# Optimization experiments

Hardware: AMD Instinct MI355X
Metric: run time of the kernel (lower is better)

Reference implementation:

```python
import jax, jax.numpy as jnp
import numpy as np

N_WAY = 5
K_SHOT = 5
NBNN_TOPK = 3
TEMPERATURE = 2.0
EPS = 1e-8


def setup_inputs() -> dict:
    key = jax.random.key(0)
    k1, k2, k3 = jax.random.split(key, 3)
    b, q, c, h, w = 4, 75, 640, 11, 11
    s = N_WAY * K_SHOT
    support_xf = jax.random.normal(k1, (b, s, c, h, w), jnp.float32)
    query_xf = jax.random.normal(k2, (b, q, c, h, w), jnp.float32)
    # episodes are ordered class-major: [way0 shots..., way1 shots..., ...]
    support_y = jnp.tile(jnp.repeat(jnp.arange(N_WAY, dtype=jnp.int32), K_SHOT)[None, :], (b, 1))
    query_y = jax.random.randint(k3, (b, q), 0, N_WAY, dtype=jnp.int32)
    return {"support_xf": support_xf, "query_xf": query_xf,
            "support_y": support_y, "query_y": query_y}


def _mn4_loss(support_xf, query_xf, query_y):
    b, s, c, h, w = support_xf.shape
    q = query_xf.shape[1]
    M_q = h * w
    M_s = K_SHOT * h * w

    # ---- InnerproductSimilarity (cosine) ----
    # support: [b, N, c, M_s]  (class-major grouping of shots)
    sf = support_xf.reshape(b, N_WAY, K_SHOT, c, h * w).transpose(0, 1, 3, 2, 4).reshape(b, N_WAY, c, M_s)
    qf = query_xf.reshape(b, q, c, M_q)
    sf = sf / (jnp.linalg.norm(sf, axis=2, keepdims=True) + EPS)
    qf = qf / (jnp.linalg.norm(qf, axis=2, keepdims=True) + EPS)
    # simi: [b, q, N, M_q, M_s]
    simi = jnp.einsum('bqcm,bncs->bqnms', qf, sf)

    # ---- _MNN (compensate_for_single=True branch) ----
    # merged view: [b, q, M_q, N*M_s]
    merged = simi.transpose(0, 1, 3, 2, 4).reshape(b, q, M_q, N_WAY * M_s)
    query_nearest = jnp.argmax(merged, axis=-1)          # [b, q, M_q]
    class_wise_max = simi.max(-1).max(2) + 1.0           # [b, q, M_q]
    class_m = jax.nn.one_hot(query_nearest, N_WAY * M_s, dtype=simi.dtype) * class_wise_max[..., None]
    support_nearest = jnp.argmax(class_m, axis=-2)       # [b, q, N*M_s]
    gathered = jnp.take_along_axis(support_nearest, query_nearest, axis=-1)  # [b, q, M_q]
    q_mask = (gathered == jnp.arange(M_q)[None, None, :])                    # [b, q, M_q]

    # ---- NBNN value: topk over support descriptors, masked sum over query descriptors ----
    topv = jax.lax.top_k(simi, NBNN_TOPK)[0].mean(-1)    # [b, q, N, M_q]
    query_value = (topv * q_mask[:, :, None, :].astype(topv.dtype)).sum(-1)  # [b, q, N]
    logits = query_value.reshape(b * q, N_WAY) / TEMPERATURE

    # ---- cross entropy (mean) ----
    logp = jax.nn.log_softmax(logits, axis=-1)
    y = query_y.reshape(-1)
    loss = -jnp.take_along_axis(logp, y[:, None], axis=1).mean()
    return loss


def reference(support_xf, query_xf, support_y, query_y):
    del support_y  # episodes are class-major by construction
    return _mn4_loss(support_xf, query_xf, query_y)
```

## Files before the change

kernel.cpp:

```cpp
#include <hip/hip_runtime.h>
#include <hip/hip_bf16.h>
#include <math.h>

#define BB 4
#define QQ 75
#define NBQ 300
#define CC 640
#define HW 121
#define NW 5
#define KS 5
#define SS 25
#define MS 605
#define JT 3025
#define BQ_PER_XCD 38

typedef __attribute__((ext_vector_type(8))) short short8;
typedef __attribute__((ext_vector_type(4))) float f32x4;

#define OFF_SBF   0
#define SBF_F     (BB*JT*CC/2)
#define OFF_QBF   (OFF_SBF + SBF_F)
#define QBF_F     (NBQ*HW*CC/2)
#define OFF_P     (OFF_QBF + QBF_F)
#define OFF_NRM   OFF_P

__device__ __forceinline__ void async16(const void* g, void* l) {
    __builtin_amdgcn_global_load_lds(
        (const __attribute__((address_space(1))) unsigned int*)g,
        (__attribute__((address_space(3))) unsigned int*)l, 16, 0, 0);
}

__global__ void norm_kernel(const float* __restrict__ sup, const float* __restrict__ qry,
                            float* __restrict__ nrm, float* __restrict__ out)
{
    const int blk = blockIdx.x;
    const int col = blk >> 2, r = blk & 3;
    const int hw  = threadIdx.x;
    if (blk == 0 && hw == 0) out[0] = 0.f;
    const float* src = (col < BB * SS)
        ? sup + (size_t)col * (CC * HW)
        : qry + (size_t)(col - BB * SS) * (CC * HW);
    float ss = 0.f;
    if (hw < HW) {
        const float* p = src + hw;
#pragma unroll 16
        for (int i = 0; i < CC / 4; ++i) {
            const float v = p[(size_t)(r + i * 4) * HW];
            ss = fmaf(v, v, ss);
        }
    }
    nrm[((size_t)col * 4 + r) * 128 + hw] = ss;
}

__global__ void scale_kernel(const float* __restrict__ sup, const float* __restrict__ qry,
                             const float* __restrict__ nrm,
                             __hip_bfloat16* __restrict__ Sbf, __hip_bfloat16* __restrict__ Qbf)
{
    const int blk = blockIdx.x;
    const int col = blk >> 2, qtr = blk & 3;
    const int t   = threadIdx.x;
    const float* src;
    __hip_bfloat16* dst;
    if (col < BB * SS) {
        const int b = col / SS, s = col % SS;
        const int n = s / KS, k = s % KS;
        src = sup + (size_t)col * (CC * HW);
        dst = Sbf + ((size_t)b * JT + n * MS + k * HW) * CC;
    } else {
        const int bq = col - BB * SS;
        src = qry + (size_t)bq * (CC * HW);
        dst = Qbf + (size_t)bq * (HW * CC);
    }

    __shared__ float inv[128];
    __shared__ float T[32][128];

    if (t < 128) {
        const float p0 = nrm[((size_t)col * 4 + 0) * 128 + t];
        const float p1 = nrm[((size_t)col * 4 + 1) * 128 + t];
        const float p2 = nrm[((size_t)col * 4 + 2) * 128 + t];
        const float p3 = nrm[((size_t)col * 4 + 3) * 128 + t];
        inv[t] = (t < HW) ? 1.f / (sqrtf((p0 + p2) + (p1 + p3)) + 1e-8f) : 0.f;
    }

    for (int it = 0; it < 5; ++it) {
        const int c0 = qtr * 160 + it * 32;
        __syncthreads();
#pragma unroll
        for (int i = 0; i < 16; ++i) {
            int idx = t + i * 256;
            int cc = idx >> 7, hw = idx & 127;
            if (hw < HW) T[cc][hw] = src[(size_t)(c0 + cc) * HW + hw] * inv[hw];
        }
        __syncthreads();
        const int hw = t >> 1, half = t & 1;
        if (hw < HW) {
            __hip_bfloat16 hv[16];
#pragma unroll
            for (int i = 0; i < 16; ++i) hv[i] = __float2bfloat16(T[half * 16 + i][hw]);
            int4* op = reinterpret_cast<int4*>(dst + (size_t)hw * CC + c0 + half * 16);
            op[0] = reinterpret_cast<int4*>(hv)[0];
            op[1] = reinterpret_cast<int4*>(hv)[1];
        }
    }
}

__launch_bounds__(256, 3)
__global__ void simi_kernel(const __hip_bfloat16* __restrict__ Sbf,
                            const __hip_bfloat16* __restrict__ Qbf,
                            float4* __restrict__ pout)
{
    const int xcd   = blockIdx.x & 7;
    const int local = blockIdx.x >> 3;
    const int n     = local % NW;
    const int bq    = xcd * BQ_PER_XCD + local / NW;
    if (bq >= NBQ) return;
    const int b   = bq / QQ;
    const int tid = threadIdx.x;
    const int lane = tid & 63, wid = tid >> 6;
    const int l15 = lane & 15, l4 = lane >> 4;
    const int wj0 = (wid & 1) * 64;
    const int wm0 = (wid >> 1) * 64;

    const unsigned short* qbase = (const unsigned short*)(Qbf + (size_t)bq * (HW * CC));
    const unsigned short* sbase = (const unsigned short*)(Sbf + ((size_t)b * JT + n * MS) * CC);

    __shared__ __align__(16) unsigned short AsBuf[3][128 * 32];
    __shared__ __align__(16) unsigned short BsBuf[3][128 * 32];

    const int srow = lane >> 2;
    const int kb   = (lane & 3) ^ ((lane >> 3) & 3);
    int aoff2[2];
#pragma unroll
    for (int g = 0; g < 2; ++g) {
        int arow = wid * 32 + g * 16 + srow;
        int grow = arow < HW ? arow : HW - 1;
        aoff2[g] = grow * CC + kb * 8;
    }
    int jb2[2];
#pragma unroll
    for (int g = 0; g < 2; ++g) jb2[g] = wid * 32 + g * 16 + srow;

    const int ldso_base = wid * 2048 + lane * 16;

#define STAGE(ms0_, c0_, nb_)                                                        \
    {                                                                                \
        _Pragma("unroll")                                                            \
        for (int g = 0; g < 2; ++g) {                                                \
            const int ldso = ldso_base + g * 1024;                                   \
            async16(qbase + aoff2[g] + (c0_), (char*)&AsBuf[nb_][0] + ldso);         \
            int j_ = (ms0_) + jb2[g];                                                \
            int jc_ = j_ < MS ? j_ : MS - 1;                                         \
            async16(sbase + jc_ * CC + kb * 8 + (c0_), (char*)&BsBuf[nb_][0] + ldso);\
        }                                                                            \
    }

    float rt0[4], rt1[4], rt2[4]; int ra[4];
#pragma unroll
    for (int i = 0; i < 4; ++i) { rt0[i] = -INFINITY; rt1[i] = -INFINITY; rt2[i] = -INFINITY; ra[i] = 0; }

    f32x4 acc[4][4];
#pragma unroll
    for (int ji = 0; ji < 4; ++ji)
#pragma unroll
        for (int qi = 0; qi < 4; ++qi)
#pragma unroll
            for (int r = 0; r < 4; ++r) acc[ji][qi][r] = 0.f;

    STAGE(0, 0, 0);
    int nb = 0;

    const int slot = l4 ^ ((l15 >> 1) & 3);
    const int aro  = (wm0 + l15) * 32 + slot * 8;
    const int bro  = (wj0 + l15) * 32 + slot * 8;

    for (int t = 0; t < 100; ++t) {
        const int tn = t + 1;
        const int nxt = (nb == 2) ? 0 : nb + 1;
        if (tn < 100) {
            const int nms = (tn / 20) * 128;
            const int nc  = (tn % 20) * 32;
            STAGE(nms, nc, nxt);
            asm volatile("s_waitcnt vmcnt(4)" ::: "memory");
        } else {
            asm volatile("s_waitcnt vmcnt(0)" ::: "memory");
        }
        __builtin_amdgcn_s_barrier();

        short8 af[4], bf[4];
#pragma unroll
        for (int qi = 0; qi < 4; ++qi)
            af[qi] = *(const short8*)(&AsBuf[nb][0] + aro + qi * 512);
#pragma unroll
        for (int ji = 0; ji < 4; ++ji)
            bf[ji] = *(const short8*)(&BsBuf[nb][0] + bro + ji * 512);

        __builtin_amdgcn_s_setprio(1);
#pragma unroll
        for (int ji = 0; ji < 4; ++ji)
#pragma unroll
            for (int qi = 0; qi < 4; ++qi)
                acc[ji][qi] = __builtin_amdgcn_mfma_f32_16x16x32_bf16(
                    bf[ji], af[qi], acc[ji][qi], 0, 0, 0);
        __builtin_amdgcn_s_setprio(0);
        nb = nxt;

        if ((t % 20) == 19) {
            const int ms0 = (t / 20) * 128;
#pragma unroll
            for (int qi = 0; qi < 4; ++qi)
#pragma unroll
                for (int ji = 0; ji < 4; ++ji)
#pragma unroll
                    for (int r = 0; r < 4; ++r) {
                        const int jl = ms0 + wj0 + ji * 16 + l4 * 4 + r;
                        float v = (jl < MS) ? acc[ji][qi][r] : -INFINITY;
                        const bool gt = v > rt0[qi];
                        ra[qi] = gt ? (n * MS + jl) : ra[qi];
                        const float m1 = fminf(rt0[qi], v);
                        rt0[qi] = fmaxf(rt0[qi], v);
                        const float m2 = fminf(rt1[qi], m1);
                        rt1[qi] = fmaxf(rt1[qi], m1);
                        rt2[qi] = fmaxf(rt2[qi], m2);
                    }
#pragma unroll
            for (int ji = 0; ji < 4; ++ji)
#pragma unroll
                for (int qi = 0; qi < 4; ++qi)
#pragma unroll
                    for (int r = 0; r < 4; ++r) acc[ji][qi][r] = 0.f;
        }
    }

#pragma unroll
    for (int qi = 0; qi < 4; ++qi) {
#pragma unroll
        for (int mask = 16; mask <= 32; mask <<= 1) {
            const float o0 = __shfl_xor(rt0[qi], mask);
            const float o1 = __shfl_xor(rt1[qi], mask);
            const float o2 = __shfl_xor(rt2[qi], mask);
            const int   oa = __shfl_xor(ra[qi],  mask);
            const bool take = (o0 > rt0[qi]) || (o0 == rt0[qi] && oa < ra[qi]);
            ra[qi] = take ? oa : ra[qi];
            float m1 = fminf(rt0[qi], o0); rt0[qi] = fmaxf(rt0[qi], o0);
            float m2 = fminf(rt1[qi], m1); rt1[qi] = fmaxf(rt1[qi], m1);
            rt2[qi] = fmaxf(rt2[qi], m2);
            m1 = fminf(rt0[qi], o1); rt0[qi] = fmaxf(rt0[qi], o1);
            m2 = fminf(rt1[qi], m1); rt1[qi] = fmaxf(rt1[qi], m1);
            rt2[qi] = fmaxf(rt2[qi], m2);
            m1 = fminf(rt0[qi], o2); rt0[qi] = fmaxf(rt0[qi], o2);
            m2 = fminf(rt1[qi], m1); rt1[qi] = fmaxf(rt1[qi], m1);
            rt2[qi] = fmaxf(rt2[qi], m2);
        }
    }

    __syncthreads();
    float4* mbuf = (float4*)&AsBuf[0][0];
    if ((wid & 1) == 0 && l4 == 0) {
#pragma unroll
        for (int qi = 0; qi < 4; ++qi) {
            float4 v; v.x = rt0[qi]; v.y = rt1[qi]; v.z = rt2[qi];
            v.w = __int_as_float(ra[qi]);
            mbuf[wm0 + qi * 16 + l15] = v;
        }
    }
    __syncthreads();
    if ((wid & 1) == 1 && l4 == 0) {
#pragma unroll
        for (int qi = 0; qi < 4; ++qi) {
            const int m = wm0 + qi * 16 + l15;
            const float4 o = mbuf[m];
            const int oa = __float_as_int(o.w);
            float s0 = rt0[qi], s1 = rt1[qi], s2 = rt2[qi]; int sa = ra[qi];
            const bool take = (o.x > s0) || (o.x == s0 && oa < sa);
            sa = take ? oa : sa;
            float m1 = fminf(s0, o.x); s0 = fmaxf(s0, o.x);
            float m2 = fminf(s1, m1);  s1 = fmaxf(s1, m1);
            s2 = fmaxf(s2, m2);
            m1 = fminf(s0, o.y); s0 = fmaxf(s0, o.y);
            m2 = fminf(s1, m1);  s1 = fmaxf(s1, m1);
            s2 = fmaxf(s2, m2);
            m1 = fminf(s0, o.z); s0 = fmaxf(s0, o.z);
            m2 = fminf(s1, m1);  s1 = fmaxf(s1, m1);
            s2 = fmaxf(s2, m2);
            if (m < HW) {
                float4 v; v.x = s0; v.y = s1; v.z = s2; v.w = __int_as_float(sa);
                pout[(bq * NW + n) * HW + m] = v;
            }
        }
    }
#undef STAGE
}

__global__ void merge_kernel(const float4* __restrict__ pout, const int* __restrict__ qy,
                             float* __restrict__ out)
{
    const int bq  = blockIdx.x;
    const int tid = threadIdx.x;

    __shared__ float cw[128];
    __shared__ int   ag[128];
    __shared__ float tv[NW][128];
    __shared__ float maskf[128];
    __shared__ float lg[8];

    if (tid < HW) {
        float g0 = -INFINITY; int garg = 0;
#pragma unroll
        for (int n = 0; n < NW; ++n) {
            const float4 a = pout[(bq * NW + n) * HW + tid];
            if (a.x > g0) { g0 = a.x; garg = __float_as_int(a.w); }
            tv[n][tid] = (a.x + a.y + a.z) * (1.f / 3.f);
        }
        cw[tid] = g0 + 1.0f;
        ag[tid] = garg;
    }
    __syncthreads();
    if (tid < HW) {
        const float mycw = cw[tid];
        const int   myag = ag[tid];
        float ok = 1.f;
        for (int m2 = 0; m2 < HW; ++m2) {
            if (m2 == tid) continue;
            if (ag[m2] == myag) {
                float c2 = cw[m2];
                if (c2 > mycw || (c2 == mycw && m2 < tid)) ok = 0.f;
            }
        }
        maskf[tid] = ok;
    }
    __syncthreads();
    if (tid < NW) {
        float s = 0.f;
        for (int mq = 0; mq < HW; ++mq) s += maskf[mq] * tv[tid][mq];
        lg[tid] = s * 0.5f;
    }
    __syncthreads();
    if (tid == 0) {
        float m = lg[0];
#pragma unroll
        for (int n2 = 1; n2 < NW; ++n2) m = fmaxf(m, lg[n2]);
        float se = 0.f;
#pragma unroll
        for (int n2 = 0; n2 < NW; ++n2) se += expf(lg[n2] - m);
        int y = qy[bq];
        atomicAdd(out, -(lg[y] - m - logf(se)) * (1.f / NBQ));
    }
}

extern "C" void kernel_launch(void* const* d_in, const int* in_sizes, int n_in,
                              void* d_out, int out_size, void* d_ws, size_t ws_size,
                              hipStream_t stream)
{
    const float* sup = (const float*)d_in[0];
    const float* qry = (const float*)d_in[1];
    const int*   qy  = (const int*)d_in[3];
    float* out = (float*)d_out;
    float* ws  = (float*)d_ws;

    __hip_bfloat16* Sbf = (__hip_bfloat16*)(ws + OFF_SBF);
    __hip_bfloat16* Qbf = (__hip_bfloat16*)(ws + OFF_QBF);
    float4* pout = (float4*)(ws + OFF_P);
    float*  nrm  = (float*)(ws + OFF_NRM);

    hipLaunchKernelGGL(norm_kernel,  dim3((BB * SS + NBQ) * 4), dim3(128), 0, stream,
                       sup, qry, nrm, out);
    hipLaunchKernelGGL(scale_kernel, dim3((BB * SS + NBQ) * 4), dim3(256), 0, stream,
                       sup, qry, nrm, Sbf, Qbf);
    hipLaunchKernelGGL(simi_kernel, dim3(8 * BQ_PER_XCD * NW), dim3(256), 0, stream,
                       Sbf, Qbf, pout);
    hipLaunchKernelGGL(merge_kernel, dim3(NBQ), dim3(128), 0, stream, pout, qy, out);
}
```

Baseline: 402.3 us.

## Process two queries per block to share support tile loads

Result: faster. 393.2 us (-2.3%).

```diff
diff --git a/kernel.cpp b/kernel.cpp
--- a/kernel.cpp
+++ b/kernel.cpp
@@ -12,7 +12,8 @@
 #define SS 25
 #define MS 605
 #define JT 3025
-#define BQ_PER_XCD 38
+#define NPAIR 38
+#define PAIRS_PER_XCD 19
 
 typedef __attribute__((ext_vector_type(8))) short short8;
 typedef __attribute__((ext_vector_type(4))) float f32x4;
@@ -105,7 +106,7 @@
     }
 }
 
-__launch_bounds__(256, 3)
+__launch_bounds__(512, 4)
 __global__ void simi_kernel(const __hip_bfloat16* __restrict__ Sbf,
                             const __hip_bfloat16* __restrict__ Qbf,
                             float4* __restrict__ pout)
@@ -113,46 +114,50 @@
     const int xcd   = blockIdx.x & 7;
     const int local = blockIdx.x >> 3;
     const int n     = local % NW;
-    const int bq    = xcd * BQ_PER_XCD + local / NW;
-    if (bq >= NBQ) return;
-    const int b   = bq / QQ;
-    const int tid = threadIdx.x;
+    const int pair  = xcd * PAIRS_PER_XCD + local / NW;
+    const int b     = pair / NPAIR;
+    const int pi    = pair % NPAIR;
+    const bool dup  = (pi == NPAIR - 1);
+    const int q0    = 2 * pi;
+    const int q1    = dup ? q0 : q0 + 1;
+    const int bq0   = b * QQ + q0;
+    const int bq1   = b * QQ + q1;
+
+    const int tid  = threadIdx.x;
     const int lane = tid & 63, wid = tid >> 6;
     const int l15 = lane & 15, l4 = lane >> 4;
+    const int wm0 = (wid >> 1) * 64;
     const int wj0 = (wid & 1) * 64;
-    const int wm0 = (wid >> 1) * 64;
-
-    const unsigned short* qbase = (const unsigned short*)(Qbf + (size_t)bq * (HW * CC));
+
+    const unsigned short* qb0 = (const unsigned short*)(Qbf + (size_t)bq0 * (HW * CC));
+    const unsigned short* qb1 = (const unsigned short*)(Qbf + (size_t)bq1 * (HW * CC));
     const unsigned short* sbase = (const unsigned short*)(Sbf + ((size_t)b * JT + n * MS) * CC);
 
-    __shared__ __align__(16) unsigned short AsBuf[3][128 * 32];
+    __shared__ __align__(16) unsigned short AsBuf[3][256 * 32];
     __shared__ __align__(16) unsigned short BsBuf[3][128 * 32];
 
     const int srow = lane >> 2;
     const int kb   = (lane & 3) ^ ((lane >> 3) & 3);
-    int aoff2[2];
+
+    const unsigned short* aptr[2];
 #pragma unroll
     for (int g = 0; g < 2; ++g) {
         int arow = wid * 32 + g * 16 + srow;
-        int grow = arow < HW ? arow : HW - 1;
-        aoff2[g] = grow * CC + kb * 8;
-    }
-    int jb2[2];
-#pragma unroll
-    for (int g = 0; g < 2; ++g) jb2[g] = wid * 32 + g * 16 + srow;
-
-    const int ldso_base = wid * 2048 + lane * 16;
+        int ml = arow & 127; ml = ml < HW ? ml : HW - 1;
+        aptr[g] = ((arow >> 7) ? qb1 : qb0) + ml * CC + kb * 8;
+    }
+    const int jrow = wid * 16 + srow;
+    const int ldsoA0 = wid * 2048 + lane * 16;
+    const int ldsoA1 = ldsoA0 + 1024;
+    const int ldsoB  = wid * 1024 + lane * 16;
 
 #define STAGE(ms0_, c0_, nb_)                                                        \
     {                                                                                \
-        _Pragma("unroll")                                                            \
-        for (int g = 0; g < 2; ++g) {                                                \
-            const int ldso = ldso_base + g * 1024;                                   \
-            async16(qbase + aoff2[g] + (c0_), (char*)&AsBuf[nb_][0] + ldso);         \
-            int j_ = (ms0_) + jb2[g];                                                \
-            int jc_ = j_ < MS ? j_ : MS - 1;                                         \
-            async16(sbase + jc_ * CC + kb * 8 + (c0_), (char*)&BsBuf[nb_][0] + ldso);\
-        }                                                                            \
+        async16(aptr[0] + (c0_), (char*)&AsBuf[nb_][0] + ldsoA0);                    \
+        async16(aptr[1] + (c0_), (char*)&AsBuf[nb_][0] + ldsoA1);                    \
+        int j_ = (ms0_) + jrow;                                                      \
+        int jc_ = j_ < MS ? j_ : MS - 1;                                             \
+        async16(sbase + jc_ * CC + kb * 8 + (c0_), (char*)&BsBuf[nb_][0] + ldsoB);   \
     }
 
     float rt0[4], rt1[4], rt2[4]; int ra[4];
@@ -181,27 +186,29 @@
             const int nms = (tn / 20) * 128;
             const int nc  = (tn % 20) * 32;
             STAGE(nms, nc, nxt);
-            asm volatile("s_waitcnt vmcnt(4)" ::: "memory");
+            asm volatile("s_waitcnt vmcnt(3)" ::: "memory");
         } else {
             asm volatile("s_waitcnt vmcnt(0)" ::: "memory");
         }
         __builtin_amdgcn_s_barrier();
 
-        short8 af[4], bf[4];
+        short8 af[4];
 #pragma unroll
         for (int qi = 0; qi < 4; ++qi)
             af[qi] = *(const short8*)(&AsBuf[nb][0] + aro + qi * 512);
-#pragma unroll
-        for (int ji = 0; ji < 4; ++ji)
-            bf[ji] = *(const short8*)(&BsBuf[nb][0] + bro + ji * 512);
-
+
+        short8 bfA = *(const short8*)(&BsBuf[nb][0] + bro);
         __builtin_amdgcn_s_setprio(1);
 #pragma unroll
-        for (int ji = 0; ji < 4; ++ji)
+        for (int ji = 0; ji < 4; ++ji) {
+            short8 bfB;
+            if (ji < 3) bfB = *(const short8*)(&BsBuf[nb][0] + bro + (ji + 1) * 512);
 #pragma unroll
             for (int qi = 0; qi < 4; ++qi)
                 acc[ji][qi] = __builtin_amdgcn_mfma_f32_16x16x32_bf16(
-                    bf[ji], af[qi], acc[ji][qi], 0, 0, 0);
+                    bfA, af[qi], acc[ji][qi], 0, 0, 0);
+            bfA = bfB;
+        }
         __builtin_amdgcn_s_setprio(0);
         nb = nxt;
 
@@ -283,9 +290,12 @@
             m1 = fminf(s0, o.z); s0 = fmaxf(s0, o.z);
             m2 = fminf(s1, m1);  s1 = fmaxf(s1, m1);
             s2 = fmaxf(s2, m2);
-            if (m < HW) {
+            const int bqs = m >> 7;
+            const int ml  = m & 127;
+            if (ml < HW && (bqs == 0 || !dup)) {
+                const int bqx = bqs ? bq1 : bq0;
                 float4 v; v.x = s0; v.y = s1; v.z = s2; v.w = __int_as_float(sa);
-                pout[(bq * NW + n) * HW + m] = v;
+                pout[(bqx * NW + n) * HW + ml] = v;
             }
         }
     }
@@ -367,7 +377,7 @@
                        sup, qry, nrm, out);
     hipLaunchKernelGGL(scale_kernel, dim3((BB * SS + NBQ) * 4), dim3(256), 0, stream,
                        sup, qry, nrm, Sbf, Qbf);
-    hipLaunchKernelGGL(simi_kernel, dim3(8 * BQ_PER_XCD * NW), dim3(256), 0, stream,
+    hipLaunchKernelGGL(simi_kernel, dim3(8 * PAIRS_PER_XCD * NW), dim3(512), 0, stream,
                        Sbf, Qbf, pout);
     hipLaunchKernelGGL(merge_kernel, dim3(NBQ), dim3(128), 0, stream, pout, qy, out);
 }
```
